# Performance work log

Measured on AMD Instinct MI355X. Metric: run time of the kernel, lower is better.

## Reference

```python
import jax, jax.numpy as jnp
import numpy as np

B, T, IN = 4, 1024, 172
D, H, FF, L, NCLS = 512, 8, 2048, 8, 1296
HD = D // H
EPS = 1e-5


def setup_inputs() -> dict:
    key = jax.random.key(0)
    ks = jax.random.split(key, 16)
    rn = lambda k, s, sc=0.02: jax.random.normal(k, s, jnp.float32) * sc
    return {
        "poses": jax.random.normal(ks[0], (B, T, IN), jnp.float32),
        "pose_w": rn(ks[1], (D, IN)), "pose_b": jnp.zeros((D,), jnp.float32),
        "in_w": rn(ks[2], (L, 3 * D, D)), "in_b": jnp.zeros((L, 3 * D), jnp.float32),
        "out_w": rn(ks[3], (L, D, D)), "out_b": jnp.zeros((L, D), jnp.float32),
        "ln1_g": jnp.ones((L, D), jnp.float32), "ln1_b": jnp.zeros((L, D), jnp.float32),
        "ffn_w1": rn(ks[4], (L, FF, D)), "ffn_b1": jnp.zeros((L, FF), jnp.float32),
        "ffn_w2": rn(ks[5], (L, D, FF)), "ffn_b2": jnp.zeros((L, D), jnp.float32),
        "ln2_g": jnp.ones((L, D), jnp.float32), "ln2_b": jnp.zeros((L, D), jnp.float32),
        "tcn1_w": rn(ks[6], (512, D, 5)), "tcn1_b": jnp.zeros((512,), jnp.float32),
        "tcn2_w": rn(ks[7], (D, 512, 5)), "tcn2_b": jnp.zeros((D,), jnp.float32),
        "fc1_w": rn(ks[8], (128, D)), "fc1_b": jnp.zeros((128,), jnp.float32),
        "fc2_w": rn(ks[9], (NCLS, 128)), "fc2_b": jnp.zeros((NCLS,), jnp.float32),
    }


def _pos_enc(seq_len, d):
    # PositionalEncoding1D: interleaved sin/cos per frequency pair
    inv_freq = 1.0 / (10000.0 ** (jnp.arange(0, d, 2, dtype=jnp.float32) / d))
    ang = jnp.arange(seq_len, dtype=jnp.float32)[:, None] * inv_freq  # [T, d/2]
    return jnp.stack([jnp.sin(ang), jnp.cos(ang)], axis=-1).reshape(seq_len, d)


def _ln(x, g, b):
    m = x.mean(-1, keepdims=True)
    v = jnp.var(x, axis=-1, keepdims=True)
    return (x - m) * jax.lax.rsqrt(v + EPS) * g + b


def _encoder_layer(x, iw, ib, ow, ob, g1, b1, w1, c1, w2, c2, g2, b2):
    # post-norm TransformerEncoderLayer, eager (non-flash) attention
    Bc, Tc, _ = x.shape
    qkv = x @ iw.T + ib                       # [B,T,3D]
    q, k, v = jnp.split(qkv, 3, axis=-1)
    q = q.reshape(Bc, Tc, H, HD)
    k = k.reshape(Bc, Tc, H, HD)
    v = v.reshape(Bc, Tc, H, HD)
    scores = jnp.einsum('bqhd,bkhd->bhqk', q, k) / jnp.sqrt(jnp.float32(HD))
    attn = jax.nn.softmax(scores, axis=-1)    # explicit weights (need_weights=True)
    o = jnp.einsum('bhqk,bkhd->bqhd', attn, v).reshape(Bc, Tc, D)
    o = o @ ow.T + ob
    x = _ln(x + o, g1, b1)
    f = jax.nn.relu(x @ w1.T + c1) @ w2.T + c2
    return _ln(x + f, g2, b2)


def _conv1d(x, w, b):  # x [B,T,C_in], w [C_out,C_in,5], pad=2
    y = jax.lax.conv_general_dilated(
        x.transpose(0, 2, 1), w, window_strides=(1,), padding=((2, 2),),
        dimension_numbers=('NCH', 'OIH', 'NCH'))
    return y.transpose(0, 2, 1) + b


def _avgpool2(x):  # kernel=2 stride=2 along time
    Bc, Tc, C = x.shape
    return x.reshape(Bc, Tc // 2, 2, C).mean(axis=2)


def reference(poses, pose_w, pose_b, in_w, in_b, out_w, out_b, ln1_g, ln1_b,
              ffn_w1, ffn_b1, ffn_w2, ffn_b2, ln2_g, ln2_b,
              tcn1_w, tcn1_b, tcn2_w, tcn2_b, fc1_w, fc1_b, fc2_w, fc2_b):
    x = poses.reshape(poses.shape[0], poses.shape[1], -1) @ pose_w.T + pose_b
    x = x + _pos_enc(x.shape[1], D)[None]

    def run_stack(h, idx):
        for i in idx:
            h = _encoder_layer(h, in_w[i], in_b[i], out_w[i], out_b[i],
                               ln1_g[i], ln1_b[i], ffn_w1[i], ffn_b1[i],
                               ffn_w2[i], ffn_b2[i], ln2_g[i], ln2_b[i])
        return h

    h = run_stack(x, (0, 1))
    h = run_stack(h, (2, 3)) + h
    h = run_stack(h, (4, 5)) + h
    h = run_stack(h, (6, 7)) + h

    h = _avgpool2(h)                 # [B,T/2,D]
    h = _conv1d(h, tcn1_w, tcn1_b)   # [B,T/2,512]
    h = _avgpool2(h)                 # [B,T/4,512]
    h = _conv1d(h, tcn2_w, tcn2_b)   # [B,T/4,D]
    h = h @ fc1_w.T + fc1_b
    logits = h @ fc2_w.T + fc2_b     # [B,T/4,num_classes]
    return logits
```

## Files before the change

kernel.cpp:

```cpp
#include <hip/hip_runtime.h>
#include <hip/hip_bf16.h>

static constexpr int kB = 4;
static constexpr int kT = 1024;
static constexpr int kIn = 172;
static constexpr int kD = 512;
static constexpr int kH = 8;
static constexpr int kHD = 64;
static constexpr int kFF = 2048;
static constexpr int kNCLS = 1296;
static constexpr float kEps = 1e-5f;

typedef __attribute__((ext_vector_type(8))) short bf16x8_t;
typedef __attribute__((ext_vector_type(4))) float f32x4_t;
typedef __attribute__((ext_vector_type(8))) unsigned short u16x8_t;
typedef __attribute__((ext_vector_type(4))) unsigned short u16x4_t;

static __device__ __forceinline__ unsigned short f2bf(float f) {
  unsigned int u = __float_as_uint(f);
  unsigned int r = (u + 0x7fffu + ((u >> 16) & 1u)) >> 16;
  return (unsigned short)r;
}

__global__ void cvt_kernel(const float* __restrict__ src, ushort* __restrict__ dst, int n8)
{
  const int i = blockIdx.x * 256 + threadIdx.x;
  if (i >= n8) return;
  const float4 a = *(const float4*)&src[i * 8];
  const float4 b = *(const float4*)&src[i * 8 + 4];
  u16x8_t t;
  t[0] = f2bf(a.x); t[1] = f2bf(a.y); t[2] = f2bf(a.z); t[3] = f2bf(a.w);
  t[4] = f2bf(b.x); t[5] = f2bf(b.y); t[6] = f2bf(b.z); t[7] = f2bf(b.w);
  *(u16x8_t*)&dst[i * 8] = t;
}

template<int MREP, int NREP>
__global__ __launch_bounds__(256) void bgemm_kernel(
    const ushort* __restrict__ A, const ushort* __restrict__ W,
    const float* __restrict__ bias, const float* __restrict__ resid,
    float* __restrict__ C, ushort* __restrict__ Cb, int M, int N, int K, int doRelu)
{
  constexpr int BM = MREP * 32, BN = NREP * 32;
  constexpr int SRD = 72;
  constexpr int TPRA = 256 / BM, CSA = 64 / TPRA, NLA = CSA / 8;
  constexpr int TPRB = 256 / BN, CSB = 64 / TPRB, NLB = CSB / 8;
  __shared__ ushort As[BM * SRD];
  __shared__ ushort Bs[BN * SRD];

  const int tid = threadIdx.x;
  int bid = blockIdx.y * gridDim.x + blockIdx.x;
  const int nwg = gridDim.x * gridDim.y;
  if ((nwg & 7) == 0) bid = (bid & 7) * (nwg >> 3) + (bid >> 3);
  const int bm = (bid / gridDim.x) * BM, bn = (bid % gridDim.x) * BN;

  const int wv = tid >> 6, lane = tid & 63;
  const int lr = lane & 15, lg = lane >> 4;
  const int wr = wv >> 1, wc = wv & 1;

  const int ra = tid / TPRA, ca = (tid % TPRA) * CSA;
  const int rb = tid / TPRB, cb = (tid % TPRB) * CSB;

  f32x4_t acc[MREP][NREP];
#pragma unroll
  for (int mr = 0; mr < MREP; ++mr)
#pragma unroll
    for (int nr = 0; nr < NREP; ++nr) acc[mr][nr] = (f32x4_t){0.f, 0.f, 0.f, 0.f};

  u16x8_t pa[NLA], pb[NLB];
  auto loadAB = [&](int k0) {
    const ushort* ap = A + (size_t)(bm + ra) * K + k0 + ca;
#pragma unroll
    for (int j = 0; j < NLA; ++j) pa[j] = *(const u16x8_t*)(ap + j * 8);
    const ushort* bp = W + (size_t)(bn + rb) * K + k0 + cb;
#pragma unroll
    for (int j = 0; j < NLB; ++j) pb[j] = *(const u16x8_t*)(bp + j * 8);
  };
  auto storeLDS = [&]() {
#pragma unroll
    for (int j = 0; j < NLA; ++j) *(u16x8_t*)&As[ra * SRD + ca + j * 8] = pa[j];
#pragma unroll
    for (int j = 0; j < NLB; ++j) *(u16x8_t*)&Bs[rb * SRD + cb + j * 8] = pb[j];
  };

  loadAB(0);
  storeLDS();
  __syncthreads();

  const int nsteps = K >> 6;
  for (int s = 0; s < nsteps; ++s) {
    const bool more = (s + 1) < nsteps;
    if (more) loadAB((s + 1) << 6);

#pragma unroll
    for (int kk = 0; kk < 2; ++kk) {
      bf16x8_t af[MREP];
#pragma unroll
      for (int mr = 0; mr < MREP; ++mr)
        af[mr] = *(const bf16x8_t*)&As[(wr * MREP * 16 + mr * 16 + lr) * SRD + kk * 32 + lg * 8];
#pragma unroll
      for (int nr = 0; nr < NREP; ++nr) {
        const bf16x8_t bf = *(const bf16x8_t*)&Bs[(wc * NREP * 16 + nr * 16 + lr) * SRD + kk * 32 + lg * 8];
#pragma unroll
        for (int mr = 0; mr < MREP; ++mr)
          acc[mr][nr] = __builtin_amdgcn_mfma_f32_16x16x32_bf16(af[mr], bf, acc[mr][nr], 0, 0, 0);
      }
    }
    __syncthreads();
    if (more) { storeLDS(); __syncthreads(); }
  }

#pragma unroll
  for (int mr = 0; mr < MREP; ++mr) {
#pragma unroll
    for (int v = 0; v < 4; ++v) {
      const int m = bm + wr * MREP * 16 + mr * 16 + lg * 4 + v;
#pragma unroll
      for (int nr = 0; nr < NREP; ++nr) {
        const int n = bn + wc * NREP * 16 + nr * 16 + lr;
        float val = acc[mr][nr][v] + bias[n];
        if (doRelu) val = fmaxf(val, 0.f);
        if (resid) val += resid[(size_t)m * N + n];
        if (C)  C[(size_t)m * N + n] = val;
        if (Cb) Cb[(size_t)m * N + n] = f2bf(val);
      }
    }
  }
}

#define GBM 64
#define GBN 64
#define GBK 16
#define LDST 68

__global__ __launch_bounds__(256) void gemm_kernel(
    const float* __restrict__ A, const float* __restrict__ W,
    const float* __restrict__ bias, const float* __restrict__ resid,
    float* __restrict__ C, int M, int N, int K, int doRelu)
{
  __shared__ __align__(16) float As[GBK][LDST];
  __shared__ __align__(16) float Ws[GBK][LDST];
  const int tid = threadIdx.x;
  const int bm = blockIdx.y * GBM;
  const int bn = blockIdx.x * GBN;
  const int tx = tid & 15, ty = tid >> 4;
  const int li = tid >> 2;
  const int lk = (tid & 3) << 2;

  float acc[4][4];
#pragma unroll
  for (int i = 0; i < 4; ++i)
#pragma unroll
    for (int j = 0; j < 4; ++j) acc[i][j] = 0.f;

  for (int k0 = 0; k0 < K; k0 += GBK) {
    float4 av = make_float4(0.f, 0.f, 0.f, 0.f);
    float4 wv = make_float4(0.f, 0.f, 0.f, 0.f);
    {
      const int m = bm + li;
      if (m < M) {
        if (k0 + lk + 4 <= K) {
          av = *(const float4*)&A[(size_t)m * K + k0 + lk];
        } else {
          float t4[4] = {0.f, 0.f, 0.f, 0.f};
          for (int c = 0; c < 4; ++c) { int k = k0 + lk + c; if (k < K) t4[c] = A[(size_t)m * K + k]; }
          av = make_float4(t4[0], t4[1], t4[2], t4[3]);
        }
      }
      const int n = bn + li;
      if (n < N) {
        if (k0 + lk + 4 <= K) {
          wv = *(const float4*)&W[(size_t)n * K + k0 + lk];
        } else {
          float t4[4] = {0.f, 0.f, 0.f, 0.f};
          for (int c = 0; c < 4; ++c) { int k = k0 + lk + c; if (k < K) t4[c] = W[(size_t)n * K + k]; }
          wv = make_float4(t4[0], t4[1], t4[2], t4[3]);
        }
      }
    }
    __syncthreads();
    As[lk + 0][li] = av.x; As[lk + 1][li] = av.y; As[lk + 2][li] = av.z; As[lk + 3][li] = av.w;
    Ws[lk + 0][li] = wv.x; Ws[lk + 1][li] = wv.y; Ws[lk + 2][li] = wv.z; Ws[lk + 3][li] = wv.w;
    __syncthreads();
#pragma unroll
    for (int kk = 0; kk < GBK; ++kk) {
      const float4 a4 = *(const float4*)&As[kk][ty << 2];
      const float4 b4 = *(const float4*)&Ws[kk][tx << 2];
      const float a[4] = {a4.x, a4.y, a4.z, a4.w};
      const float b[4] = {b4.x, b4.y, b4.z, b4.w};
#pragma unroll
      for (int i = 0; i < 4; ++i)
#pragma unroll
        for (int j = 0; j < 4; ++j) acc[i][j] = fmaf(a[i], b[j], acc[i][j]);
    }
  }

#pragma unroll
  for (int i = 0; i < 4; ++i) {
    const int m = bm + (ty << 2) + i;
    if (m >= M) continue;
#pragma unroll
    for (int j = 0; j < 4; ++j) {
      const int n = bn + (tx << 2) + j;
      if (n >= N) continue;
      float v = acc[i][j] + bias[n];
      if (doRelu) v = fmaxf(v, 0.f);
      if (resid) v += resid[(size_t)m * N + n];
      C[(size_t)m * N + n] = v;
    }
  }
}

__global__ __launch_bounds__(256) void ln_kernel(
    float* __restrict__ X, ushort* __restrict__ Xb,
    const float* __restrict__ g, const float* __restrict__ bta)
{
  const int row = blockIdx.x;
  const int tid = threadIdx.x;
  float* xr = X + (size_t)row * kD;
  const float x0 = xr[tid];
  const float x1 = xr[tid + 256];
  float s = x0 + x1;
  float q = x0 * x0 + x1 * x1;
#pragma unroll
  for (int off = 32; off > 0; off >>= 1) {
    s += __shfl_down(s, off);
    q += __shfl_down(q, off);
  }
  __shared__ float ss[4], qq[4];
  const int w = tid >> 6;
  if ((tid & 63) == 0) { ss[w] = s; qq[w] = q; }
  __syncthreads();
  const float S = ss[0] + ss[1] + ss[2] + ss[3];
  const float Q = qq[0] + qq[1] + qq[2] + qq[3];
  const float mean = S * (1.f / kD);
  const float var = Q * (1.f / kD) - mean * mean;
  const float inv = rsqrtf(var + kEps);
  const float v0 = (x0 - mean) * inv * g[tid] + bta[tid];
  const float v1 = (x1 - mean) * inv * g[tid + 256] + bta[tid + 256];
  xr[tid] = v0; xr[tid + 256] = v1;
  ushort* xb = Xb + (size_t)row * kD;
  xb[tid] = f2bf(v0); xb[tid + 256] = f2bf(v1);
}

#define KSTR 72
__global__ __launch_bounds__(256) void attn_mfma_kernel(
    const ushort* __restrict__ qkv, ushort* __restrict__ O)
{
  const int b = blockIdx.z, h = blockIdx.y;
  const int q0 = blockIdx.x << 6;
  const int tid = threadIdx.x;
  const int wv = tid >> 6, lane = tid & 63;
  const int lr = lane & 15;
  const int lg = lane >> 4;

  __shared__ ushort Ks[64 * KSTR];
  __shared__ ushort Vt[64 * KSTR];
  __shared__ ushort Pl[4][16 * KSTR];

  bf16x8_t qa[2];
  {
    const ushort* qrow = qkv + ((size_t)(b * kT + q0 + wv * 16 + lr)) * (3 * kD) + h * kHD + lg * 8;
    qa[0] = *(const bf16x8_t*)qrow;
    qa[1] = *(const bf16x8_t*)(qrow + 32);
  }

  float m_[4], l_[4];
  f32x4_t oacc[4];
#pragma unroll
  for (int r = 0; r < 4; ++r) { m_[r] = -1e30f; l_[r] = 0.f; }
#pragma unroll
  for (int nb = 0; nb < 4; ++nb) oacc[nb] = (f32x4_t){0.f, 0.f, 0.f, 0.f};

  const int srow = tid >> 2;
  const int sd   = (tid & 3) << 4;

  for (int kt = 0; kt < kT / 64; ++kt) {
    __syncthreads();
    {
      const ushort* kr = qkv + ((size_t)(b * kT + (kt << 6) + srow)) * (3 * kD) + kD + h * kHD + sd;
      *(u16x8_t*)&Ks[srow * KSTR + sd]     = *(const u16x8_t*)kr;
      *(u16x8_t*)&Ks[srow * KSTR + sd + 8] = *(const u16x8_t*)(kr + 8);
      const ushort* vr = kr + kD;
      const u16x8_t v0 = *(const u16x8_t*)vr;
      const u16x8_t v1 = *(const u16x8_t*)(vr + 8);
#pragma unroll
      for (int e = 0; e < 8; ++e) {
        Vt[(sd + e) * KSTR + srow] = v0[e];
        Vt[(sd + 8 + e) * KSTR + srow] = v1[e];
      }
    }
    __syncthreads();

    f32x4_t s[4];
#pragma unroll
    for (int cc = 0; cc < 4; ++cc) {
      const ushort* kb = &Ks[(cc * 16 + lr) * KSTR + lg * 8];
      const bf16x8_t k0 = *(const bf16x8_t*)kb;
      const bf16x8_t k1 = *(const bf16x8_t*)(kb + 32);
      f32x4_t acc = (f32x4_t){0.f, 0.f, 0.f, 0.f};
      acc = __builtin_amdgcn_mfma_f32_16x16x32_bf16(qa[0], k0, acc, 0, 0, 0);
      acc = __builtin_amdgcn_mfma_f32_16x16x32_bf16(qa[1], k1, acc, 0, 0, 0);
#pragma unroll
      for (int r = 0; r < 4; ++r) acc[r] *= 0.125f;
      s[cc] = acc;
    }

#pragma unroll
    for (int r = 0; r < 4; ++r) {
      float mx = fmaxf(fmaxf(s[0][r], s[1][r]), fmaxf(s[2][r], s[3][r]));
      mx = fmaxf(mx, __shfl_xor(mx, 1));
      mx = fmaxf(mx, __shfl_xor(mx, 2));
      mx = fmaxf(mx, __shfl_xor(mx, 4));
      mx = fmaxf(mx, __shfl_xor(mx, 8));
      const float mnew = fmaxf(m_[r], mx);
      const float alpha = __expf(m_[r] - mnew);
      float sum = 0.f;
#pragma unroll
      for (int cc = 0; cc < 4; ++cc) {
        const float p = __expf(s[cc][r] - mnew);
        s[cc][r] = p;
        sum += p;
      }
      sum += __shfl_xor(sum, 1);
      sum += __shfl_xor(sum, 2);
      sum += __shfl_xor(sum, 4);
      sum += __shfl_xor(sum, 8);
      l_[r] = l_[r] * alpha + sum;
      m_[r] = mnew;
#pragma unroll
      for (int nb = 0; nb < 4; ++nb) oacc[nb][r] *= alpha;
#pragma unroll
      for (int cc = 0; cc < 4; ++cc)
        Pl[wv][(lg * 4 + r) * KSTR + cc * 16 + lr] = f2bf(s[cc][r]);
    }

    const bf16x8_t pa0 = *(const bf16x8_t*)&Pl[wv][lr * KSTR + lg * 8];
    const bf16x8_t pa1 = *(const bf16x8_t*)&Pl[wv][lr * KSTR + 32 + lg * 8];
#pragma unroll
    for (int nb = 0; nb < 4; ++nb) {
      const ushort* vb = &Vt[(nb * 16 + lr) * KSTR + lg * 8];
      const bf16x8_t v0 = *(const bf16x8_t*)vb;
      const bf16x8_t v1 = *(const bf16x8_t*)(vb + 32);
      oacc[nb] = __builtin_amdgcn_mfma_f32_16x16x32_bf16(pa0, v0, oacc[nb], 0, 0, 0);
      oacc[nb] = __builtin_amdgcn_mfma_f32_16x16x32_bf16(pa1, v1, oacc[nb], 0, 0, 0);
    }
  }

#pragma unroll
  for (int nb = 0; nb < 4; ++nb) {
#pragma unroll
    for (int r = 0; r < 4; ++r) {
      const int row = lg * 4 + r;
      const int col = nb * 16 + lr;
      O[((size_t)(b * kT + q0 + wv * 16 + row)) * kD + h * kHD + col] = f2bf(oacc[nb][r] / l_[r]);
    }
  }
}

__global__ __launch_bounds__(256) void posenc_kernel(float* __restrict__ X, ushort* __restrict__ Xb)
{
  const int bt = blockIdx.x;
  const int t = bt & (kT - 1);
  float* row = X + (size_t)bt * kD;
  ushort* rb = Xb + (size_t)bt * kD;
#pragma unroll
  for (int p = 0; p < 2; ++p) {
    const int d = threadIdx.x + p * 256;
    const int j = d >> 1;
    const float inv = expf(-(float)j * 0.03597789207803197f);
    const float ang = (float)t * inv;
    const float pe = (d & 1) ? cosf(ang) : sinf(ang);
    const float v = row[d] + pe;
    row[d] = v;
    rb[d] = f2bf(v);
  }
}

__global__ void im2col_pool_kernel(const float* __restrict__ X, ushort* __restrict__ X5,
                                   int Tt, int n4)
{
  const int idx = blockIdx.x * 256 + threadIdx.x;
  if (idx >= n4) return;
  const int ci4 = idx & 127;
  int r = idx >> 7;
  const int tap = r % 5; r /= 5;
  const int t = r % Tt;
  const int b = r / Tt;
  const int ts = t + tap - 2;
  u16x4_t o = (u16x4_t){0, 0, 0, 0};
  if (ts >= 0 && ts < Tt) {
    const float* p = X + ((size_t)(b * 2 * Tt + 2 * ts)) * kD + ci4 * 4;
    const float4 x0 = *(const float4*)p;
    const float4 x1 = *(const float4*)(p + kD);
    o[0] = f2bf(0.5f * (x0.x + x1.x)); o[1] = f2bf(0.5f * (x0.y + x1.y));
    o[2] = f2bf(0.5f * (x0.z + x1.z)); o[3] = f2bf(0.5f * (x0.w + x1.w));
  }
  *(u16x4_t*)&X5[((size_t)(b * Tt + t)) * 2560 + tap * kD + ci4 * 4] = o;
}

__global__ void convw_t_kernel(const float* __restrict__ w, ushort* __restrict__ Wt)
{
  const int idx = blockIdx.x * 256 + threadIdx.x;
  if (idx >= 512 * 512 * 5) return;
  const int ci = idx & 511;
  int r = idx >> 9;
  const int tap = r % 5;
  const int co = r / 5;
  Wt[(size_t)co * 2560 + tap * 512 + ci] = f2bf(w[(size_t)co * 2560 + ci * 5 + tap]);
}

__global__ void copy_kernel(const float* __restrict__ X, float* __restrict__ Y2, int n)
{
  const int i = blockIdx.x * 256 + threadIdx.x;
  if (i < n) Y2[i] = X[i];
}
__global__ void add_dual_kernel(float* __restrict__ A, ushort* __restrict__ Ab,
                                const float* __restrict__ P, int n)
{
  const int i = blockIdx.x * 256 + threadIdx.x;
  if (i >= n) return;
  const float v = A[i] + P[i];
  A[i] = v;
  Ab[i] = f2bf(v);
}

extern "C" void kernel_launch(void* const* d_in, const int* in_sizes, int n_in,
                              void* d_out, int out_size, void* d_ws, size_t ws_size,
                              hipStream_t stream)
{
  (void)in_sizes; (void)n_in; (void)out_size;
  const float* poses  = (const float*)d_in[0];
  const float* pose_w = (const float*)d_in[1];
  const float* pose_b = (const float*)d_in[2];
  const float* in_w   = (const float*)d_in[3];
  const float* in_b   = (const float*)d_in[4];
  const float* out_w  = (const float*)d_in[5];
  const float* out_b  = (const float*)d_in[6];
  const float* ln1_g  = (const float*)d_in[7];
  const float* ln1_b  = (const float*)d_in[8];
  const float* ffn_w1 = (const float*)d_in[9];
  const float* ffn_b1 = (const float*)d_in[10];
  const float* ffn_w2 = (const float*)d_in[11];
  const float* ffn_b2 = (const float*)d_in[12];
  const float* ln2_g  = (const float*)d_in[13];
  const float* ln2_b  = (const float*)d_in[14];
  const float* tcn1_w = (const float*)d_in[15];
  const float* tcn1_b = (const float*)d_in[16];
  const float* tcn2_w = (const float*)d_in[17];
  const float* tcn2_b = (const float*)d_in[18];
  const float* fc1_w  = (const float*)d_in[19];
  const float* fc1_b  = (const float*)d_in[20];
  const float* fc2_w  = (const float*)d_in[21];
  const float* fc2_b  = (const float*)d_in[22];

  char* base = (char*)d_ws;
  const size_t SZ = (size_t)kB * kT * kD;
  float*  A    = (float*)(base);
  float*  Y    = (float*)(base + 8388608);
  float*  P    = (float*)(base + 16777216);
  ushort* Abf  = (ushort*)(base + 25165824);
  ushort* QKV  = (ushort*)(base + 29360128);
  ushort* Ybf  = QKV;
  ushort* X5   = QKV;
  ushort* MID  = (ushort*)(base + 41943040);
  ushort* ATTb = MID;
  ushort* CW   = MID;
  ushort* Wbf  = (ushort*)(base + 58720256);

  const size_t nWq = (size_t)3 * kD * kD;
  const size_t nWo = (size_t)kD * kD;
  const size_t nW1 = (size_t)kFF * kD;
  const size_t nW2 = (size_t)kD * kFF;
  const size_t nWl = nWq + nWo + nW1 + nW2;
  const bool fullW = ws_size >= (size_t)58720256 + nWl * 8 * 2;

  const int M = kB * kT;
  dim3 blk(256);
  auto cvt = [&](const float* s, ushort* d, size_t n) {
    cvt_kernel<<<(int)((n / 8 + 255) / 256), blk, 0, stream>>>(s, d, (int)(n / 8));
  };

  if (fullW) {
    cvt(in_w,   Wbf,                        nWq * 8);
    cvt(out_w,  Wbf + nWq * 8,              nWo * 8);
    cvt(ffn_w1, Wbf + nWq * 8 + nWo * 8,    nW1 * 8);
    cvt(ffn_w2, Wbf + (nWq + nWo + nW1) * 8, nW2 * 8);
  }

  gemm_kernel<<<dim3(kD / GBN, M / GBM), blk, 0, stream>>>(poses, pose_w, pose_b, nullptr, A, M, kD, kIn, 0);
  posenc_kernel<<<M, blk, 0, stream>>>(A, Abf);

  for (int l = 0; l < 8; ++l) {
    const ushort *Wq, *Wo, *W1, *W2;
    if (fullW) {
      Wq = Wbf + (size_t)l * nWq;
      Wo = Wbf + nWq * 8 + (size_t)l * nWo;
      W1 = Wbf + nWq * 8 + nWo * 8 + (size_t)l * nW1;
      W2 = Wbf + (nWq + nWo + nW1) * 8 + (size_t)l * nW2;
    } else {
      cvt(in_w   + (size_t)l * nWq, Wbf, nWq);
      cvt(out_w  + (size_t)l * nWo, Wbf + nWq, nWo);
      cvt(ffn_w1 + (size_t)l * nW1, Wbf + nWq + nWo, nW1);
      cvt(ffn_w2 + (size_t)l * nW2, Wbf + nWq + nWo + nW1, nW2);
      Wq = Wbf; Wo = Wbf + nWq; W1 = Wbf + nWq + nWo; W2 = Wbf + nWq + nWo + nW1;
    }

    if (l == 2 || l == 4 || l == 6)
      copy_kernel<<<(int)(SZ / 256), blk, 0, stream>>>(A, P, (int)SZ);

    bgemm_kernel<4, 4><<<dim3(3 * kD / 128, M / 128), blk, 0, stream>>>(
        Abf, Wq, in_b + (size_t)l * 3 * kD, nullptr, nullptr, QKV, M, 3 * kD, kD, 0);
    attn_mfma_kernel<<<dim3(kT / 64, kH, kB), blk, 0, stream>>>(QKV, ATTb);
    bgemm_kernel<2, 4><<<dim3(kD / 128, M / 64), blk, 0, stream>>>(
        ATTb, Wo, out_b + (size_t)l * kD, A, Y, nullptr, M, kD, kD, 0);
    ln_kernel<<<M, blk, 0, stream>>>(Y, Ybf, ln1_g + (size_t)l * kD, ln1_b + (size_t)l * kD);
    bgemm_kernel<4, 4><<<dim3(kFF / 128, M / 128), blk, 0, stream>>>(
        Ybf, W1, ffn_b1 + (size_t)l * kFF, nullptr, nullptr, MID, M, kFF, kD, 1);
    bgemm_kernel<2, 4><<<dim3(kD / 128, M / 64), blk, 0, stream>>>(
        MID, W2, ffn_b2 + (size_t)l * kD, Y, A, nullptr, M, kD, kFF, 0);
    ln_kernel<<<M, blk, 0, stream>>>(A, Abf, ln2_g + (size_t)l * kD, ln2_b + (size_t)l * kD);

    if (l == 3 || l == 5 || l == 7)
      add_dual_kernel<<<(int)(SZ / 256), blk, 0, stream>>>(A, Abf, P, (int)SZ);
  }

  {
    const int T1 = kT / 2;
    const int T2 = kT / 4;
    convw_t_kernel<<<(512 * 512 * 5 + 255) / 256, blk, 0, stream>>>(tcn1_w, CW);
    const int n4a = kB * T1 * 5 * (kD / 4);
    im2col_pool_kernel<<<(n4a + 255) / 256, blk, 0, stream>>>(A, X5, T1, n4a);
    bgemm_kernel<2, 2><<<dim3(kD / 64, kB * T1 / 64), blk, 0, stream>>>(
        X5, CW, tcn1_b, nullptr, Y, nullptr, kB * T1, kD, 2560, 0);
    convw_t_kernel<<<(512 * 512 * 5 + 255) / 256, blk, 0, stream>>>(tcn2_w, CW);
    const int n4b = kB * T2 * 5 * (kD / 4);
    im2col_pool_kernel<<<(n4b + 255) / 256, blk, 0, stream>>>(Y, X5, T2, n4b);
    bgemm_kernel<2, 2><<<dim3(kD / 64, kB * T2 / 64), blk, 0, stream>>>(
        X5, CW, tcn2_b, nullptr, A, nullptr, kB * T2, kD, 2560, 0);
    const int Mh = kB * T2;
    gemm_kernel<<<dim3(128 / GBN, Mh / GBM), blk, 0, stream>>>(A, fc1_w, fc1_b, nullptr, Y, Mh, 128, kD, 0);
    gemm_kernel<<<dim3((kNCLS + GBN - 1) / GBN, Mh / GBM), blk, 0, stream>>>(
        Y, fc2_w, fc2_b, nullptr, (float*)d_out, Mh, kNCLS, 128, 0);
  }
}
```

Measured before the change: 1.500 ms.

## Fuse residual snapshot/add into LayerNorm and fix attention LDS bank conflicts

```diff
diff --git a/kernel.cpp b/kernel.cpp
--- a/kernel.cpp
+++ b/kernel.cpp
@@ -212,7 +212,8 @@
 
 __global__ __launch_bounds__(256) void ln_kernel(
     float* __restrict__ X, ushort* __restrict__ Xb,
-    const float* __restrict__ g, const float* __restrict__ bta)
+    const float* __restrict__ g, const float* __restrict__ bta,
+    const float* Padd, float* Pout)
 {
   const int row = blockIdx.x;
   const int tid = threadIdx.x;
@@ -235,14 +236,23 @@
   const float mean = S * (1.f / kD);
   const float var = Q * (1.f / kD) - mean * mean;
   const float inv = rsqrtf(var + kEps);
-  const float v0 = (x0 - mean) * inv * g[tid] + bta[tid];
-  const float v1 = (x1 - mean) * inv * g[tid + 256] + bta[tid + 256];
+  float v0 = (x0 - mean) * inv * g[tid] + bta[tid];
+  float v1 = (x1 - mean) * inv * g[tid + 256] + bta[tid + 256];
+  if (Padd) {
+    v0 += Padd[(size_t)row * kD + tid];
+    v1 += Padd[(size_t)row * kD + tid + 256];
+  }
   xr[tid] = v0; xr[tid + 256] = v1;
   ushort* xb = Xb + (size_t)row * kD;
   xb[tid] = f2bf(v0); xb[tid + 256] = f2bf(v1);
+  if (Pout) {
+    Pout[(size_t)row * kD + tid] = v0;
+    Pout[(size_t)row * kD + tid + 256] = v1;
+  }
 }
 
 #define KSTR 72
+#define PSTR 74
 __global__ __launch_bounds__(256) void attn_mfma_kernel(
     const ushort* __restrict__ qkv, ushort* __restrict__ O)
 {
@@ -255,7 +265,7 @@
 
   __shared__ ushort Ks[64 * KSTR];
   __shared__ ushort Vt[64 * KSTR];
-  __shared__ ushort Pl[4][16 * KSTR];
+  __shared__ ushort Pl[4][16 * PSTR];
 
   bf16x8_t qa[2];
   {
@@ -273,6 +283,8 @@
 
   const int srow = tid >> 2;
   const int sd   = (tid & 3) << 4;
+  const int vkp  = tid & 31;
+  const int vdh  = tid >> 5;
 
   for (int kt = 0; kt < kT / 64; ++kt) {
     __syncthreads();
@@ -280,13 +292,13 @@
       const ushort* kr = qkv + ((size_t)(b * kT + (kt << 6) + srow)) * (3 * kD) + kD + h * kHD + sd;
       *(u16x8_t*)&Ks[srow * KSTR + sd]     = *(const u16x8_t*)kr;
       *(u16x8_t*)&Ks[srow * KSTR + sd + 8] = *(const u16x8_t*)(kr + 8);
-      const ushort* vr = kr + kD;
+      const ushort* vr = qkv + ((size_t)(b * kT + (kt << 6) + 2 * vkp)) * (3 * kD) + 2 * kD + h * kHD + vdh * 8;
       const u16x8_t v0 = *(const u16x8_t*)vr;
-      const u16x8_t v1 = *(const u16x8_t*)(vr + 8);
+      const u16x8_t v1 = *(const u16x8_t*)(vr + 3 * kD);
 #pragma unroll
       for (int e = 0; e < 8; ++e) {
-        Vt[(sd + e) * KSTR + srow] = v0[e];
-        Vt[(sd + 8 + e) * KSTR + srow] = v1[e];
+        const unsigned int packv = (unsigned int)v0[e] | ((unsigned int)v1[e] << 16);
+        *(unsigned int*)&Vt[(vdh * 8 + e) * KSTR + 2 * vkp] = packv;
       }
     }
     __syncthreads();
@@ -331,11 +343,11 @@
       for (int nb = 0; nb < 4; ++nb) oacc[nb][r] *= alpha;
 #pragma unroll
       for (int cc = 0; cc < 4; ++cc)
-        Pl[wv][(lg * 4 + r) * KSTR + cc * 16 + lr] = f2bf(s[cc][r]);
-    }
-
-    const bf16x8_t pa0 = *(const bf16x8_t*)&Pl[wv][lr * KSTR + lg * 8];
-    const bf16x8_t pa1 = *(const bf16x8_t*)&Pl[wv][lr * KSTR + 32 + lg * 8];
+        Pl[wv][(lg * 4 + r) * PSTR + cc * 16 + lr] = f2bf(s[cc][r]);
+    }
+
+    const bf16x8_t pa0 = *(const bf16x8_t*)&Pl[wv][lr * PSTR + lg * 8];
+    const bf16x8_t pa1 = *(const bf16x8_t*)&Pl[wv][lr * PSTR + 32 + lg * 8];
 #pragma unroll
     for (int nb = 0; nb < 4; ++nb) {
       const ushort* vb = &Vt[(nb * 16 + lr) * KSTR + lg * 8];
@@ -407,21 +419,6 @@
   const int tap = r % 5;
   const int co = r / 5;
   Wt[(size_t)co * 2560 + tap * 512 + ci] = f2bf(w[(size_t)co * 2560 + ci * 5 + tap]);
-}
-
-__global__ void copy_kernel(const float* __restrict__ X, float* __restrict__ Y2, int n)
-{
-  const int i = blockIdx.x * 256 + threadIdx.x;
-  if (i < n) Y2[i] = X[i];
-}
-__global__ void add_dual_kernel(float* __restrict__ A, ushort* __restrict__ Ab,
-                                const float* __restrict__ P, int n)
-{
-  const int i = blockIdx.x * 256 + threadIdx.x;
-  if (i >= n) return;
-  const float v = A[i] + P[i];
-  A[i] = v;
-  Ab[i] = f2bf(v);
 }
 
 extern "C" void kernel_launch(void* const* d_in, const int* in_sizes, int n_in,
@@ -454,7 +451,6 @@
   const float* fc2_b  = (const float*)d_in[22];
 
   char* base = (char*)d_ws;
-  const size_t SZ = (size_t)kB * kT * kD;
   float*  A    = (float*)(base);
   float*  Y    = (float*)(base + 8388608);
   float*  P    = (float*)(base + 16777216);
@@ -505,23 +501,23 @@
       Wq = Wbf; Wo = Wbf + nWq; W1 = Wbf + nWq + nWo; W2 = Wbf + nWq + nWo + nW1;
     }
 
-    if (l == 2 || l == 4 || l == 6)
-      copy_kernel<<<(int)(SZ / 256), blk, 0, stream>>>(A, P, (int)SZ);
-
     bgemm_kernel<4, 4><<<dim3(3 * kD / 128, M / 128), blk, 0, stream>>>(
         Abf, Wq, in_b + (size_t)l * 3 * kD, nullptr, nullptr, QKV, M, 3 * kD, kD, 0);
     attn_mfma_kernel<<<dim3(kT / 64, kH, kB), blk, 0, stream>>>(QKV, ATTb);
     bgemm_kernel<2, 4><<<dim3(kD / 128, M / 64), blk, 0, stream>>>(
         ATTb, Wo, out_b + (size_t)l * kD, A, Y, nullptr, M, kD, kD, 0);
-    ln_kernel<<<M, blk, 0, stream>>>(Y, Ybf, ln1_g + (size_t)l * kD, ln1_b + (size_t)l * kD);
+    ln_kernel<<<M, blk, 0, stream>>>(Y, Ybf, ln1_g + (size_t)l * kD, ln1_b + (size_t)l * kD,
+                                     nullptr, nullptr);
     bgemm_kernel<4, 4><<<dim3(kFF / 128, M / 128), blk, 0, stream>>>(
         Ybf, W1, ffn_b1 + (size_t)l * kFF, nullptr, nullptr, MID, M, kFF, kD, 1);
     bgemm_kernel<2, 4><<<dim3(kD / 128, M / 64), blk, 0, stream>>>(
         MID, W2, ffn_b2 + (size_t)l * kD, Y, A, nullptr, M, kD, kFF, 0);
-    ln_kernel<<<M, blk, 0, stream>>>(A, Abf, ln2_g + (size_t)l * kD, ln2_b + (size_t)l * kD);
-
-    if (l == 3 || l == 5 || l == 7)
-      add_dual_kernel<<<(int)(SZ / 256), blk, 0, stream>>>(A, Abf, P, (int)SZ);
+    {
+      const float* padd = (l == 3 || l == 5 || l == 7) ? P : nullptr;
+      float* pout = (l == 1 || l == 3 || l == 5) ? P : nullptr;
+      ln_kernel<<<M, blk, 0, stream>>>(A, Abf, ln2_g + (size_t)l * kD, ln2_b + (size_t)l * kD,
+                                       padd, pout);
+    }
   }
 
   {
```

Result: faster. 1.458 ms (-2.8%).
